# Optimization experiments

Measured on AMD Instinct MI355X. Metric: run time of the kernel, lower is better.

## Reference

```python
import jax, jax.numpy as jnp
import numpy as np
from jax import lax

N_VOX = 100000   # occupied voxels
GRID = 160       # dense grid extent per axis
K = 5            # kernel size -> 125 offsets
K3 = K * K * K
IMG_C, PTS_C, OUT_C = 64, 32, 16
EPS = 1e-5


def _build_coords_and_kernel_map():
    """Random unique voxel coords + kernel map: nbr[n,k] = row index of voxel at
    coords[n]+offset[k], or N_VOX (sentinel -> zero feature) if unoccupied."""
    rng = np.random.default_rng(0)
    flat = rng.choice(GRID ** 3, size=N_VOX, replace=False)
    coords = np.stack(np.unravel_index(flat, (GRID, GRID, GRID)), axis=1).astype(np.int64)
    B = GRID + 4  # shift coords by +2 so offsets in [-2,2] never wrap
    enc = ((coords[:, 0] + 2) * B + (coords[:, 1] + 2)) * B + (coords[:, 2] + 2)
    order = np.argsort(enc)
    enc_s = enc[order]
    offs = np.stack(np.meshgrid(np.arange(-2, 3), np.arange(-2, 3), np.arange(-2, 3), indexing='ij'), axis=-1).reshape(-1, 3)
    nbr = np.full((N_VOX, K3), N_VOX, dtype=np.int32)
    for k, (dx, dy, dz) in enumerate(offs):
        qe = enc + ((dx * B + dy) * B + dz)
        pos = np.clip(np.searchsorted(enc_s, qe), 0, N_VOX - 1)
        hit = enc_s[pos] == qe
        nbr[:, k] = np.where(hit, order[pos].astype(np.int32), np.int32(N_VOX))
    return nbr


def setup_inputs() -> dict:
    nbr_idx = jnp.asarray(_build_coords_and_kernel_map())
    key = jax.random.key(0)
    ks = jax.random.split(key, 20)
    def w(k, shape, fan):
        return jax.random.normal(k, shape, jnp.float32) * (1.0 / np.sqrt(fan))
    def bn(k0, k1, k2, k3):
        g = jax.random.uniform(k0, (OUT_C,), jnp.float32) + 0.5
        b = jax.random.normal(k1, (OUT_C,), jnp.float32) * 0.1
        m = jax.random.normal(k2, (OUT_C,), jnp.float32) * 0.1
        v = jax.random.uniform(k3, (OUT_C,), jnp.float32) + 0.5
        return g, b, m, v
    bn_img = bn(ks[2], ks[3], ks[4], ks[5])
    bn_pts = bn(ks[7], ks[8], ks[9], ks[10])
    bn_vis = bn(ks[12], ks[13], ks[14], ks[15])
    return {
        'img_voxel_feats': jax.random.normal(ks[0], (N_VOX, IMG_C), jnp.float32),
        'pts_voxel_feats': jax.random.normal(ks[1], (N_VOX, PTS_C), jnp.float32),
        'nbr_idx': nbr_idx,
        'W_img': w(ks[16], (K3, IMG_C, OUT_C), K3 * IMG_C),
        'bn_img_g': bn_img[0], 'bn_img_b': bn_img[1], 'bn_img_m': bn_img[2], 'bn_img_v': bn_img[3],
        'W_pts': w(ks[17], (K3, PTS_C, OUT_C), K3 * PTS_C),
        'bn_pts_g': bn_pts[0], 'bn_pts_b': bn_pts[1], 'bn_pts_m': bn_pts[2], 'bn_pts_v': bn_pts[3],
        'W_vis1': w(ks[18], (K3, 2 * OUT_C, OUT_C), K3 * 2 * OUT_C),
        'bn_vis_g': bn_vis[0], 'bn_vis_b': bn_vis[1], 'bn_vis_m': bn_vis[2], 'bn_vis_v': bn_vis[3],
        'W_vis2': w(ks[19], (OUT_C, 1), OUT_C),
    }


def _sparse_conv(feats, W, nbr_idx):
    # gather-GEMM-scatter sparse conv; sentinel row N -> zero feature
    feats_pad = jnp.concatenate([feats, jnp.zeros((1, feats.shape[1]), feats.dtype)], axis=0)
    init = jnp.zeros((feats.shape[0], W.shape[2]), feats.dtype)
    def step(acc, wk_ik):
        W_k, idx_k = wk_ik  # [Cin,Cout], [N]
        return acc + feats_pad[idx_k] @ W_k, None
    out, _ = lax.scan(step, init, (W, nbr_idx.T))
    return out


def _bn_relu(x, g, b, m, v):
    return jax.nn.relu((x - m) * (g * lax.rsqrt(v + EPS)) + b)


def reference(img_voxel_feats, pts_voxel_feats, nbr_idx,
              W_img, bn_img_g, bn_img_b, bn_img_m, bn_img_v,
              W_pts, bn_pts_g, bn_pts_b, bn_pts_m, bn_pts_v,
              W_vis1, bn_vis_g, bn_vis_b, bn_vis_m, bn_vis_v,
              W_vis2):
    img = _bn_relu(_sparse_conv(img_voxel_feats, W_img, nbr_idx), bn_img_g, bn_img_b, bn_img_m, bn_img_v)
    pts = _bn_relu(_sparse_conv(pts_voxel_feats, W_pts, nbr_idx), bn_pts_g, bn_pts_b, bn_pts_m, bn_pts_v)
    cat = jnp.concatenate([img, pts], axis=1)  # [N, 2*OUT_C]
    h = _bn_relu(_sparse_conv(cat, W_vis1, nbr_idx), bn_vis_g, bn_vis_b, bn_vis_m, bn_vis_v)
    vis_w = jax.nn.sigmoid(h @ W_vis2)  # [N,1]
    return vis_w * img + (1.0 - vis_w) * pts
```

## Files before the change

### kernel.cpp

```cpp
#include <hip/hip_runtime.h>

#define N_VOX 100000
#define K3 125
#define CENTER_K 62
#define CAP 4096
#define EPSF 1e-5f

#define CNT 0
#define PRS 2048
#define ACC (2048 + 2 * 125 * CAP)
#define ACV (ACC + N_VOX * 32)
#define CAT (ACV + N_VOX * 16)

__global__ __launch_bounds__(256) void prep(float* __restrict__ ws)
{
    float4 z = make_float4(0.f, 0.f, 0.f, 0.f);
    float4* w4 = (float4*)ws;
    const int NCNT4 = 2048 / 4;
    const int NACC4 = (N_VOX * 48) / 4;
    const int ACC4 = ACC / 4;
    for (int i = blockIdx.x * 256 + threadIdx.x; i < NCNT4 + NACC4; i += gridDim.x * 256)
        w4[i < NCNT4 ? i : ACC4 + (i - NCNT4)] = z;
}

__global__ __launch_bounds__(256) void build_pairs(const int* __restrict__ nbr,
                                                   float* __restrict__ ws)
{
    int* cnt = (int*)(ws + CNT);
    int2* pairs = (int2*)(ws + PRS);
    const int TOT = N_VOX * K3;
    for (int i = blockIdx.x * 256 + threadIdx.x; i < TOT; i += gridDim.x * 256) {
        int idx = nbr[i];
        int k = i % K3;
        if (idx < N_VOX && k != CENTER_K) {
            int n = i / K3;
            int pos = atomicAdd(&cnt[k * 16], 1);
            if (pos < CAP) pairs[k * CAP + pos] = make_int2(n, idx);
        }
    }
}

__global__ __launch_bounds__(256) void scatterA(
    const float* __restrict__ fimg, const float* __restrict__ fpts,
    const float* __restrict__ Wimg, const float* __restrict__ Wpts,
    float* __restrict__ ws)
{
    int k = blockIdx.x;
    int o = threadIdx.x & 15;
    int slot = threadIdx.x >> 4;
    float Wi_r[64];
    #pragma unroll
    for (int c = 0; c < 64; ++c) Wi_r[c] = Wimg[k * 1024 + c * 16 + o];
    float Wp_r[32];
    #pragma unroll
    for (int c = 0; c < 32; ++c) Wp_r[c] = Wpts[k * 512 + c * 16 + o];

    int cnt = ((const int*)(ws + CNT))[k * 16];
    if (cnt > CAP) cnt = CAP;
    const int2* __restrict__ pairs = (const int2*)(ws + PRS) + (size_t)k * CAP;
    float* __restrict__ acc = ws + ACC;
    const float4* __restrict__ fi4 = (const float4*)fimg;
    const float4* __restrict__ fp4 = (const float4*)fpts;

    for (int p = blockIdx.y * 16 + slot; p < cnt; p += gridDim.y * 16) {
        int2 pr = pairs[p];
        const float4* fr = fi4 + (size_t)pr.y * 16;
        const float4* gr = fp4 + (size_t)pr.y * 8;
        float aI = 0.f, aP = 0.f;
        #pragma unroll
        for (int t = 0; t < 16; ++t) {
            float4 f = fr[t];
            aI += f.x * Wi_r[4*t] + f.y * Wi_r[4*t+1] + f.z * Wi_r[4*t+2] + f.w * Wi_r[4*t+3];
        }
        #pragma unroll
        for (int t = 0; t < 8; ++t) {
            float4 f = gr[t];
            aP += f.x * Wp_r[4*t] + f.y * Wp_r[4*t+1] + f.z * Wp_r[4*t+2] + f.w * Wp_r[4*t+3];
        }
        atomicAdd(&acc[(size_t)pr.x * 32 + o], aI);
        atomicAdd(&acc[(size_t)pr.x * 32 + 16 + o], aP);
    }
}

__global__ __launch_bounds__(256) void finalizeA(
    const float* __restrict__ fimg, const float* __restrict__ fpts,
    const float* __restrict__ Wimg, const float* __restrict__ Wpts,
    float* __restrict__ ws,
    const float* __restrict__ gi, const float* __restrict__ bi,
    const float* __restrict__ mi, const float* __restrict__ vi,
    const float* __restrict__ gp, const float* __restrict__ bp,
    const float* __restrict__ mp, const float* __restrict__ vp)
{
    int o = threadIdx.x & 15;
    int slot = threadIdx.x >> 4;
    float Wi_r[64];
    #pragma unroll
    for (int c = 0; c < 64; ++c) Wi_r[c] = Wimg[CENTER_K * 1024 + c * 16 + o];
    float Wp_r[32];
    #pragma unroll
    for (int c = 0; c < 32; ++c) Wp_r[c] = Wpts[CENTER_K * 512 + c * 16 + o];
    float sI = gi[o] * rsqrtf(vi[o] + EPSF), bI = bi[o], mI = mi[o];
    float sP = gp[o] * rsqrtf(vp[o] + EPSF), bP = bp[o], mP = mp[o];

    const float4* __restrict__ fi4 = (const float4*)fimg;
    const float4* __restrict__ fp4 = (const float4*)fpts;
    const float* __restrict__ acc = ws + ACC;
    float* __restrict__ cat = ws + CAT;

    for (int n = blockIdx.x * 16 + slot; n < N_VOX; n += gridDim.x * 16) {
        const float4* fr = fi4 + (size_t)n * 16;
        const float4* gr = fp4 + (size_t)n * 8;
        float aI = 0.f, aP = 0.f;
        #pragma unroll
        for (int t = 0; t < 16; ++t) {
            float4 f = fr[t];
            aI += f.x * Wi_r[4*t] + f.y * Wi_r[4*t+1] + f.z * Wi_r[4*t+2] + f.w * Wi_r[4*t+3];
        }
        #pragma unroll
        for (int t = 0; t < 8; ++t) {
            float4 f = gr[t];
            aP += f.x * Wp_r[4*t] + f.y * Wp_r[4*t+1] + f.z * Wp_r[4*t+2] + f.w * Wp_r[4*t+3];
        }
        float tI = acc[(size_t)n * 32 + o] + aI;
        float tP = acc[(size_t)n * 32 + 16 + o] + aP;
        cat[(size_t)n * 32 + o]      = fmaxf((tI - mI) * sI + bI, 0.f);
        cat[(size_t)n * 32 + 16 + o] = fmaxf((tP - mP) * sP + bP, 0.f);
    }
}

__global__ __launch_bounds__(256) void scatterV(
    const float* __restrict__ Wvis, float* __restrict__ ws)
{
    int k = blockIdx.x;
    int o = threadIdx.x & 15;
    int slot = threadIdx.x >> 4;
    float Wv_r[32];
    #pragma unroll
    for (int c = 0; c < 32; ++c) Wv_r[c] = Wvis[k * 512 + c * 16 + o];

    int cnt = ((const int*)(ws + CNT))[k * 16];
    if (cnt > CAP) cnt = CAP;
    const int2* __restrict__ pairs = (const int2*)(ws + PRS) + (size_t)k * CAP;
    const float4* __restrict__ c4 = (const float4*)(ws + CAT);
    float* __restrict__ accV = ws + ACV;

    for (int p = blockIdx.y * 16 + slot; p < cnt; p += gridDim.y * 16) {
        int2 pr = pairs[p];
        const float4* cr = c4 + (size_t)pr.y * 8;
        float aV = 0.f;
        #pragma unroll
        for (int t = 0; t < 8; ++t) {
            float4 f = cr[t];
            aV += f.x * Wv_r[4*t] + f.y * Wv_r[4*t+1] + f.z * Wv_r[4*t+2] + f.w * Wv_r[4*t+3];
        }
        atomicAdd(&accV[(size_t)pr.x * 16 + o], aV);
    }
}

__global__ __launch_bounds__(256) void finalizeB(
    const float* __restrict__ Wvis, float* __restrict__ ws,
    const float* __restrict__ gv, const float* __restrict__ bv,
    const float* __restrict__ mv, const float* __restrict__ vv,
    const float* __restrict__ w2, float* __restrict__ out)
{
    int o = threadIdx.x & 15;
    int slot = threadIdx.x >> 4;
    float Wv_r[32];
    #pragma unroll
    for (int c = 0; c < 32; ++c) Wv_r[c] = Wvis[CENTER_K * 512 + c * 16 + o];
    float sV = gv[o] * rsqrtf(vv[o] + EPSF), bV = bv[o], mV = mv[o], w2_ = w2[o];

    const float4* __restrict__ c4 = (const float4*)(ws + CAT);
    const float* __restrict__ cat = ws + CAT;
    const float* __restrict__ accV = ws + ACV;

    for (int n = blockIdx.x * 16 + slot; n < N_VOX; n += gridDim.x * 16) {
        const float4* cr = c4 + (size_t)n * 8;
        float aV = 0.f;
        #pragma unroll
        for (int t = 0; t < 8; ++t) {
            float4 f = cr[t];
            aV += f.x * Wv_r[4*t] + f.y * Wv_r[4*t+1] + f.z * Wv_r[4*t+2] + f.w * Wv_r[4*t+3];
        }
        float tV = accV[(size_t)n * 16 + o] + aV;
        float h = fmaxf((tV - mV) * sV + bV, 0.f);
        float ph = h * w2_;
        ph += __shfl_xor(ph, 1); ph += __shfl_xor(ph, 2);
        ph += __shfl_xor(ph, 4); ph += __shfl_xor(ph, 8);
        float vis = 1.f / (1.f + expf(-ph));
        float xi = cat[(size_t)n * 32 + o];
        float xp = cat[(size_t)n * 32 + 16 + o];
        out[(size_t)n * 16 + o] = vis * xi + (1.f - vis) * xp;
    }
}

extern "C" void kernel_launch(void* const* d_in, const int* in_sizes, int n_in,
                              void* d_out, int out_size, void* d_ws, size_t ws_size,
                              hipStream_t stream) {
    const float* fimg = (const float*)d_in[0];
    const float* fpts = (const float*)d_in[1];
    const int*   nbr  = (const int*)d_in[2];
    const float* Wimg = (const float*)d_in[3];
    const float* gi = (const float*)d_in[4];
    const float* bi = (const float*)d_in[5];
    const float* mi = (const float*)d_in[6];
    const float* vi = (const float*)d_in[7];
    const float* Wpts = (const float*)d_in[8];
    const float* gp = (const float*)d_in[9];
    const float* bp = (const float*)d_in[10];
    const float* mp = (const float*)d_in[11];
    const float* vp = (const float*)d_in[12];
    const float* Wvis = (const float*)d_in[13];
    const float* gv = (const float*)d_in[14];
    const float* bv = (const float*)d_in[15];
    const float* mv = (const float*)d_in[16];
    const float* vv = (const float*)d_in[17];
    const float* w2 = (const float*)d_in[18];
    float* out = (float*)d_out;
    float* ws = (float*)d_ws;

    hipLaunchKernelGGL(prep, dim3(1024), dim3(256), 0, stream, ws);
    hipLaunchKernelGGL(build_pairs, dim3(3072), dim3(256), 0, stream, nbr, ws);
    hipLaunchKernelGGL(scatterA, dim3(125, 16), dim3(256), 0, stream,
                       fimg, fpts, Wimg, Wpts, ws);
    hipLaunchKernelGGL(finalizeA, dim3(1024), dim3(256), 0, stream,
                       fimg, fpts, Wimg, Wpts, ws, gi, bi, mi, vi, gp, bp, mp, vp);
    hipLaunchKernelGGL(scatterV, dim3(125, 16), dim3(256), 0, stream, Wvis, ws);
    hipLaunchKernelGGL(finalizeB, dim3(1024), dim3(256), 0, stream,
                       Wvis, ws, gv, bv, mv, vv, w2, out);
}
```

Measured before the change: 202.2 us.

## Vectorize pair building, software-pipeline scatter gathers, split channel reduction, use memset

Several changes land at once. build_pairs now reads the neighbor map as int4, and the zeroing kernel is replaced with two hipMemsetAsync calls. scatterA and scatterV are rewritten with double-buffered register prefetch of the next pair's features, and scatterA splits the input channels across half-waves with a shuffle reduction so each lane issues one atomic instead of two. The dot-product accumulators in the finalize kernels are split into two chains for ILP, and grid sizes are retuned. The new code uses more registers and adds memset API calls.

```diff
diff --git a/kernel.cpp b/kernel.cpp
--- a/kernel.cpp
+++ b/kernel.cpp
@@ -12,32 +12,61 @@
 #define ACV (ACC + N_VOX * 32)
 #define CAT (ACV + N_VOX * 16)
 
-__global__ __launch_bounds__(256) void prep(float* __restrict__ ws)
-{
-    float4 z = make_float4(0.f, 0.f, 0.f, 0.f);
-    float4* w4 = (float4*)ws;
-    const int NCNT4 = 2048 / 4;
-    const int NACC4 = (N_VOX * 48) / 4;
-    const int ACC4 = ACC / 4;
-    for (int i = blockIdx.x * 256 + threadIdx.x; i < NCNT4 + NACC4; i += gridDim.x * 256)
-        w4[i < NCNT4 ? i : ACC4 + (i - NCNT4)] = z;
-}
-
 __global__ __launch_bounds__(256) void build_pairs(const int* __restrict__ nbr,
                                                    float* __restrict__ ws)
 {
     int* cnt = (int*)(ws + CNT);
     int2* pairs = (int2*)(ws + PRS);
-    const int TOT = N_VOX * K3;
-    for (int i = blockIdx.x * 256 + threadIdx.x; i < TOT; i += gridDim.x * 256) {
-        int idx = nbr[i];
-        int k = i % K3;
-        if (idx < N_VOX && k != CENTER_K) {
+    const int TOT4 = (N_VOX * K3) / 4;
+    const int4* n4 = (const int4*)nbr;
+    for (int i4 = blockIdx.x * 256 + threadIdx.x; i4 < TOT4; i4 += gridDim.x * 256) {
+        int4 v = n4[i4];
+        int base = i4 * 4;
+        int idxs[4] = {v.x, v.y, v.z, v.w};
+        #pragma unroll
+        for (int j = 0; j < 4; ++j) {
+            int idx = idxs[j];
+            int i = base + j;
             int n = i / K3;
-            int pos = atomicAdd(&cnt[k * 16], 1);
-            if (pos < CAP) pairs[k * CAP + pos] = make_int2(n, idx);
-        }
-    }
+            int k = i - n * K3;
+            if (idx < N_VOX && k != CENTER_K) {
+                int pos = atomicAdd(&cnt[k * 16], 1);
+                if (pos < CAP) pairs[(size_t)k * CAP + pos] = make_int2(n, idx);
+            }
+        }
+    }
+}
+
+__device__ __forceinline__ void loadFA(float4 (&F)[12], int2 pr,
+    const float4* __restrict__ fi4, const float4* __restrict__ fp4, int h)
+{
+    const float4* fi = fi4 + (size_t)pr.y * 16 + h * 8;
+    const float4* fp = fp4 + (size_t)pr.y * 8 + h * 4;
+    #pragma unroll
+    for (int j = 0; j < 8; ++j) F[j] = fi[j];
+    #pragma unroll
+    for (int j = 0; j < 4; ++j) F[8 + j] = fp[j];
+}
+
+__device__ __forceinline__ void computeFA(const float4 (&F)[12],
+    const float (&Wi)[32], const float (&Wp)[16], float& aI, float& aP)
+{
+    float a0 = 0.f, a1 = 0.f, b0 = 0.f, b1 = 0.f;
+    #pragma unroll
+    for (int j = 0; j < 4; ++j) {
+        float4 f = F[j];
+        a0 += f.x*Wi[4*j] + f.y*Wi[4*j+1] + f.z*Wi[4*j+2] + f.w*Wi[4*j+3];
+        float4 g = F[4 + j];
+        a1 += g.x*Wi[16+4*j] + g.y*Wi[16+4*j+1] + g.z*Wi[16+4*j+2] + g.w*Wi[16+4*j+3];
+    }
+    #pragma unroll
+    for (int j = 0; j < 2; ++j) {
+        float4 f = F[8 + j];
+        b0 += f.x*Wp[4*j] + f.y*Wp[4*j+1] + f.z*Wp[4*j+2] + f.w*Wp[4*j+3];
+        float4 g = F[10 + j];
+        b1 += g.x*Wp[8+4*j] + g.y*Wp[8+4*j+1] + g.z*Wp[8+4*j+2] + g.w*Wp[8+4*j+3];
+    }
+    aI = a0 + a1; aP = b0 + b1;
 }
 
 __global__ __launch_bounds__(256) void scatterA(
@@ -45,15 +74,19 @@
     const float* __restrict__ Wimg, const float* __restrict__ Wpts,
     float* __restrict__ ws)
 {
-    int k = blockIdx.x;
-    int o = threadIdx.x & 15;
-    int slot = threadIdx.x >> 4;
-    float Wi_r[64];
-    #pragma unroll
-    for (int c = 0; c < 64; ++c) Wi_r[c] = Wimg[k * 1024 + c * 16 + o];
-    float Wp_r[32];
-    #pragma unroll
-    for (int c = 0; c < 32; ++c) Wp_r[c] = Wpts[k * 512 + c * 16 + o];
+    const int k = blockIdx.x;
+    const int lane = threadIdx.x & 63;
+    const int wv = threadIdx.x >> 6;
+    const int s = lane >> 5;
+    const int h = (lane >> 4) & 1;
+    const int o = lane & 15;
+
+    float Wi[32];
+    #pragma unroll
+    for (int j = 0; j < 32; ++j) Wi[j] = Wimg[k * 1024 + (h * 32 + j) * 16 + o];
+    float Wp[16];
+    #pragma unroll
+    for (int j = 0; j < 16; ++j) Wp[j] = Wpts[k * 512 + (h * 16 + j) * 16 + o];
 
     int cnt = ((const int*)(ws + CNT))[k * 16];
     if (cnt > CAP) cnt = CAP;
@@ -62,23 +95,108 @@
     const float4* __restrict__ fi4 = (const float4*)fimg;
     const float4* __restrict__ fp4 = (const float4*)fpts;
 
-    for (int p = blockIdx.y * 16 + slot; p < cnt; p += gridDim.y * 16) {
-        int2 pr = pairs[p];
-        const float4* fr = fi4 + (size_t)pr.y * 16;
-        const float4* gr = fp4 + (size_t)pr.y * 8;
-        float aI = 0.f, aP = 0.f;
-        #pragma unroll
-        for (int t = 0; t < 16; ++t) {
-            float4 f = fr[t];
-            aI += f.x * Wi_r[4*t] + f.y * Wi_r[4*t+1] + f.z * Wi_r[4*t+2] + f.w * Wi_r[4*t+3];
-        }
-        #pragma unroll
-        for (int t = 0; t < 8; ++t) {
-            float4 f = gr[t];
-            aP += f.x * Wp_r[4*t] + f.y * Wp_r[4*t+1] + f.z * Wp_r[4*t+2] + f.w * Wp_r[4*t+3];
-        }
-        atomicAdd(&acc[(size_t)pr.x * 32 + o], aI);
-        atomicAdd(&acc[(size_t)pr.x * 32 + 16 + o], aP);
+    const int S = gridDim.y * 8;
+    int p = (blockIdx.y * 4 + wv) * 2 + s;
+
+    int2 prA = make_int2(0, 0), prB = make_int2(0, 0);
+    if (p < cnt) prA = pairs[p];
+    if (p + S < cnt) prB = pairs[p + S];
+    float4 FA[12], FB[12];
+    loadFA(FA, prA, fi4, fp4, h);
+
+    while (p < cnt) {
+        {
+            int2 prC = make_int2(0, 0);
+            if (p + 2 * S < cnt) prC = pairs[p + 2 * S];
+            loadFA(FB, prB, fi4, fp4, h);
+            float aI, aP;
+            computeFA(FA, Wi, Wp, aI, aP);
+            aI += __shfl_xor(aI, 16); aP += __shfl_xor(aP, 16);
+            atomicAdd(&acc[(size_t)prA.x * 32 + h * 16 + o], h ? aP : aI);
+            p += S; prA = prB; prB = prC;
+        }
+        if (p >= cnt) break;
+        {
+            int2 prC = make_int2(0, 0);
+            if (p + 2 * S < cnt) prC = pairs[p + 2 * S];
+            loadFA(FA, prB, fi4, fp4, h);
+            float aI, aP;
+            computeFA(FB, Wi, Wp, aI, aP);
+            aI += __shfl_xor(aI, 16); aP += __shfl_xor(aP, 16);
+            atomicAdd(&acc[(size_t)prA.x * 32 + h * 16 + o], h ? aP : aI);
+            p += S; prA = prB; prB = prC;
+        }
+    }
+}
+
+__device__ __forceinline__ void loadFV(float4 (&F)[8], int2 pr,
+    const float4* __restrict__ c4)
+{
+    const float4* cr = c4 + (size_t)pr.y * 8;
+    #pragma unroll
+    for (int j = 0; j < 8; ++j) F[j] = cr[j];
+}
+
+__device__ __forceinline__ void computeFV(const float4 (&F)[8],
+    const float (&Wv)[32], float& aV)
+{
+    float a0 = 0.f, a1 = 0.f;
+    #pragma unroll
+    for (int j = 0; j < 4; ++j) {
+        float4 f = F[j];
+        a0 += f.x*Wv[4*j] + f.y*Wv[4*j+1] + f.z*Wv[4*j+2] + f.w*Wv[4*j+3];
+        float4 g = F[4 + j];
+        a1 += g.x*Wv[16+4*j] + g.y*Wv[16+4*j+1] + g.z*Wv[16+4*j+2] + g.w*Wv[16+4*j+3];
+    }
+    aV = a0 + a1;
+}
+
+__global__ __launch_bounds__(256) void scatterV(
+    const float* __restrict__ Wvis, float* __restrict__ ws)
+{
+    const int k = blockIdx.x;
+    const int lane = threadIdx.x & 63;
+    const int wv = threadIdx.x >> 6;
+    const int s = lane >> 4;
+    const int o = lane & 15;
+
+    float Wv[32];
+    #pragma unroll
+    for (int j = 0; j < 32; ++j) Wv[j] = Wvis[k * 512 + j * 16 + o];
+
+    int cnt = ((const int*)(ws + CNT))[k * 16];
+    if (cnt > CAP) cnt = CAP;
+    const int2* __restrict__ pairs = (const int2*)(ws + PRS) + (size_t)k * CAP;
+    const float4* __restrict__ c4 = (const float4*)(ws + CAT);
+    float* __restrict__ accV = ws + ACV;
+
+    const int S = gridDim.y * 16;
+    int p = (blockIdx.y * 4 + wv) * 4 + s;
+
+    int2 prA = make_int2(0, 0), prB = make_int2(0, 0);
+    if (p < cnt) prA = pairs[p];
+    if (p + S < cnt) prB = pairs[p + S];
+    float4 FA[8], FB[8];
+    loadFV(FA, prA, c4);
+
+    while (p < cnt) {
+        {
+            int2 prC = make_int2(0, 0);
+            if (p + 2 * S < cnt) prC = pairs[p + 2 * S];
+            loadFV(FB, prB, c4);
+            float aV; computeFV(FA, Wv, aV);
+            atomicAdd(&accV[(size_t)prA.x * 16 + o], aV);
+            p += S; prA = prB; prB = prC;
+        }
+        if (p >= cnt) break;
+        {
+            int2 prC = make_int2(0, 0);
+            if (p + 2 * S < cnt) prC = pairs[p + 2 * S];
+            loadFV(FA, prB, c4);
+            float aV; computeFV(FB, Wv, aV);
+            atomicAdd(&accV[(size_t)prA.x * 16 + o], aV);
+            p += S; prA = prB; prB = prC;
+        }
     }
 }
 
@@ -110,50 +228,25 @@
     for (int n = blockIdx.x * 16 + slot; n < N_VOX; n += gridDim.x * 16) {
         const float4* fr = fi4 + (size_t)n * 16;
         const float4* gr = fp4 + (size_t)n * 8;
-        float aI = 0.f, aP = 0.f;
-        #pragma unroll
-        for (int t = 0; t < 16; ++t) {
-            float4 f = fr[t];
-            aI += f.x * Wi_r[4*t] + f.y * Wi_r[4*t+1] + f.z * Wi_r[4*t+2] + f.w * Wi_r[4*t+3];
-        }
+        float aI0 = 0.f, aI1 = 0.f, aP0 = 0.f, aP1 = 0.f;
         #pragma unroll
         for (int t = 0; t < 8; ++t) {
+            float4 f = fr[t];
+            aI0 += f.x*Wi_r[4*t] + f.y*Wi_r[4*t+1] + f.z*Wi_r[4*t+2] + f.w*Wi_r[4*t+3];
+            float4 g = fr[8 + t];
+            aI1 += g.x*Wi_r[32+4*t] + g.y*Wi_r[32+4*t+1] + g.z*Wi_r[32+4*t+2] + g.w*Wi_r[32+4*t+3];
+        }
+        #pragma unroll
+        for (int t = 0; t < 4; ++t) {
             float4 f = gr[t];
-            aP += f.x * Wp_r[4*t] + f.y * Wp_r[4*t+1] + f.z * Wp_r[4*t+2] + f.w * Wp_r[4*t+3];
-        }
-        float tI = acc[(size_t)n * 32 + o] + aI;
-        float tP = acc[(size_t)n * 32 + 16 + o] + aP;
+            aP0 += f.x*Wp_r[4*t] + f.y*Wp_r[4*t+1] + f.z*Wp_r[4*t+2] + f.w*Wp_r[4*t+3];
+            float4 g = gr[4 + t];
+            aP1 += g.x*Wp_r[16+4*t] + g.y*Wp_r[16+4*t+1] + g.z*Wp_r[16+4*t+2] + g.w*Wp_r[16+4*t+3];
+        }
+        float tI = acc[(size_t)n * 32 + o] + aI0 + aI1;
+        float tP = acc[(size_t)n * 32 + 16 + o] + aP0 + aP1;
         cat[(size_t)n * 32 + o]      = fmaxf((tI - mI) * sI + bI, 0.f);
         cat[(size_t)n * 32 + 16 + o] = fmaxf((tP - mP) * sP + bP, 0.f);
-    }
-}
-
-__global__ __launch_bounds__(256) void scatterV(
-    const float* __restrict__ Wvis, float* __restrict__ ws)
-{
-    int k = blockIdx.x;
-    int o = threadIdx.x & 15;
-    int slot = threadIdx.x >> 4;
-    float Wv_r[32];
-    #pragma unroll
-    for (int c = 0; c < 32; ++c) Wv_r[c] = Wvis[k * 512 + c * 16 + o];
-
-    int cnt = ((const int*)(ws + CNT))[k * 16];
-    if (cnt > CAP) cnt = CAP;
-    const int2* __restrict__ pairs = (const int2*)(ws + PRS) + (size_t)k * CAP;
-    const float4* __restrict__ c4 = (const float4*)(ws + CAT);
-    float* __restrict__ accV = ws + ACV;
-
-    for (int p = blockIdx.y * 16 + slot; p < cnt; p += gridDim.y * 16) {
-        int2 pr = pairs[p];
-        const float4* cr = c4 + (size_t)pr.y * 8;
-        float aV = 0.f;
-        #pragma unroll
-        for (int t = 0; t < 8; ++t) {
-            float4 f = cr[t];
-            aV += f.x * Wv_r[4*t] + f.y * Wv_r[4*t+1] + f.z * Wv_r[4*t+2] + f.w * Wv_r[4*t+3];
-        }
-        atomicAdd(&accV[(size_t)pr.x * 16 + o], aV);
     }
 }
 
@@ -176,13 +269,15 @@
 
     for (int n = blockIdx.x * 16 + slot; n < N_VOX; n += gridDim.x * 16) {
         const float4* cr = c4 + (size_t)n * 8;
-        float aV = 0.f;
+        float a0 = 0.f, a1 = 0.f;
         #pragma unroll
-        for (int t = 0; t < 8; ++t) {
+        for (int t = 0; t < 4; ++t) {
             float4 f = cr[t];
-            aV += f.x * Wv_r[4*t] + f.y * Wv_r[4*t+1] + f.z * Wv_r[4*t+2] + f.w * Wv_r[4*t+3];
-        }
-        float tV = accV[(size_t)n * 16 + o] + aV;
+            a0 += f.x*Wv_r[4*t] + f.y*Wv_r[4*t+1] + f.z*Wv_r[4*t+2] + f.w*Wv_r[4*t+3];
+            float4 g = cr[4 + t];
+            a1 += g.x*Wv_r[16+4*t] + g.y*Wv_r[16+4*t+1] + g.z*Wv_r[16+4*t+2] + g.w*Wv_r[16+4*t+3];
+        }
+        float tV = accV[(size_t)n * 16 + o] + a0 + a1;
         float h = fmaxf((tV - mV) * sV + bV, 0.f);
         float ph = h * w2_;
         ph += __shfl_xor(ph, 1); ph += __shfl_xor(ph, 2);
@@ -219,13 +314,15 @@
     float* out = (float*)d_out;
     float* ws = (float*)d_ws;
 
-    hipLaunchKernelGGL(prep, dim3(1024), dim3(256), 0, stream, ws);
-    hipLaunchKernelGGL(build_pairs, dim3(3072), dim3(256), 0, stream, nbr, ws);
-    hipLaunchKernelGGL(scatterA, dim3(125, 16), dim3(256), 0, stream,
+    hipMemsetAsync(ws + CNT, 0, 2048 * sizeof(float), stream);
+    hipMemsetAsync(ws + ACC, 0, (size_t)N_VOX * 48 * sizeof(float), stream);
+
+    hipLaunchKernelGGL(build_pairs, dim3(4096), dim3(256), 0, stream, nbr, ws);
+    hipLaunchKernelGGL(scatterA, dim3(125, 8), dim3(256), 0, stream,
                        fimg, fpts, Wimg, Wpts, ws);
     hipLaunchKernelGGL(finalizeA, dim3(1024), dim3(256), 0, stream,
                        fimg, fpts, Wimg, Wpts, ws, gi, bi, mi, vi, gp, bp, mp, vp);
-    hipLaunchKernelGGL(scatterV, dim3(125, 16), dim3(256), 0, stream, Wvis, ws);
+    hipLaunchKernelGGL(scatterV, dim3(125, 8), dim3(256), 0, stream, Wvis, ws);
     hipLaunchKernelGGL(finalizeB, dim3(1024), dim3(256), 0, stream,
                        Wvis, ws, gv, bv, mv, vv, w2, out);
 }
```

Result: no change. 205.6 us (+1.7%).
